# Optimization experiments

Measured on AMD Instinct MI355X. Metric: run time of the kernel, lower is better.

## Reference

```python
import math
import jax, jax.numpy as jnp
import numpy as np

NUM_HEADS = 12
HIDDEN = 768
HEAD_DIM = HIDDEN // NUM_HEADS
BS, SEQ = 4, 2048


def setup_inputs() -> dict:
    key = jax.random.key(0)
    ks = jax.random.split(key, 8)
    hidden_states = jax.random.normal(ks[0], (BS, SEQ, HIDDEN), dtype=jnp.float32)
    attention_mask = jax.random.normal(ks[1], (BS, 1, 1, SEQ), dtype=jnp.float32)
    scale = 0.02
    Wq = jax.random.normal(ks[2], (HIDDEN, HIDDEN), dtype=jnp.float32) * scale
    Wk = jax.random.normal(ks[3], (HIDDEN, HIDDEN), dtype=jnp.float32) * scale
    Wv = jax.random.normal(ks[4], (HIDDEN, HIDDEN), dtype=jnp.float32) * scale
    bq = jax.random.normal(ks[5], (HIDDEN,), dtype=jnp.float32) * scale
    bk = jax.random.normal(ks[6], (HIDDEN,), dtype=jnp.float32) * scale
    bv = jax.random.normal(ks[7], (HIDDEN,), dtype=jnp.float32) * scale
    return {"hidden_states": hidden_states, "attention_mask": attention_mask,
            "Wq": Wq, "bq": bq, "Wk": Wk, "bk": bk, "Wv": Wv, "bv": bv}


def reference(hidden_states, attention_mask, Wq, bq, Wk, bk, Wv, bv):
    B, S, H = hidden_states.shape
    nh, hd = NUM_HEADS, H // NUM_HEADS

    def transform(W, b):
        # [B,S,H] -> [B,nh,S,hd]  (nn.Linear: x @ W.T + b, then view+transpose)
        p = hidden_states @ W.T + b
        return p.reshape(B, S, nh, hd).transpose(0, 2, 1, 3)

    q = transform(Wq, bq)
    k = transform(Wk, bk)
    v = transform(Wv, bv)

    # scores: [B, nh, S, S], scaled by sqrt(head_dim)
    scores = jnp.einsum('bhqd,bhkd->bhqk', q, k) / math.sqrt(hd)
    # masked_fill(attention_mask < 0, -10000); mask broadcasts [B,1,1,S]
    scores = jnp.where(attention_mask < 0, jnp.float32(-10000.0), scores)
    probs = jax.nn.softmax(scores, axis=-1)
    per_head = jnp.einsum('bhqk,bhkd->bhqd', probs, v)
    # cat over heads along last dim == transpose back and merge head dims
    return per_head.transpose(0, 2, 1, 3).reshape(B, S, H)
```

## Files before the change

kernel.cpp:

```cpp
#include <hip/hip_runtime.h>

typedef __attribute__((ext_vector_type(8))) __bf16 bf16x8;
typedef __attribute__((ext_vector_type(4))) __bf16 bf16x4;
typedef __attribute__((ext_vector_type(4))) float f32x4;

#define NB 4
#define SEQ 2048
#define HID 768
#define NH 12
#define HD 64
#define NC 1280

#define MFMA(a,b,c) __builtin_amdgcn_mfma_f32_16x16x32_bf16(a, b, c, 0, 0, 0)

__global__ __launch_bounds__(256) void prep_kernel(
    const float* __restrict__ mask, const float* __restrict__ X,
    const float* __restrict__ Wq, const float* __restrict__ Wk,
    const float* __restrict__ Wv,
    int* __restrict__ idx, int* __restrict__ counts,
    __bf16* __restrict__ Xb, __bf16* __restrict__ Wb) {
  int blk = blockIdx.x;
  if (blk < NB) {
    int lane = threadIdx.x;
    if (lane < 64) {
      int b = blk;
      int base = 0;
      for (int c = 0; c < SEQ / 64; c++) {
        float mv = mask[b * SEQ + c * 64 + lane];
        unsigned long long ball = __ballot(mv >= 0.0f);
        int pre = __popcll(ball & ((1ull << lane) - 1ull));
        if (mv >= 0.0f) idx[b * SEQ + base + pre] = c * 64 + lane;
        base += (int)__popcll(ball);
      }
      if (lane == 0) counts[b] = base;
    }
    return;
  }
  const long NX = (long)NB * SEQ * HID;
  const long NW = (long)HID * HID;
  long i8 = ((long)(blk - NB) * 256 + threadIdx.x) * 8;
  const float* src;
  __bf16* dst;
  if (i8 < NX) {
    src = X + i8; dst = Xb + i8;
  } else {
    long j = i8 - NX;
    int w = (int)(j / NW);
    long r = j - (long)w * NW;
    src = (w == 0 ? Wq : (w == 1 ? Wk : Wv)) + r;
    dst = Wb + j;
  }
  const float4* s4 = (const float4*)src;
  float4 a = s4[0], b = s4[1];
  bf16x8 v;
  v[0] = (__bf16)a.x; v[1] = (__bf16)a.y; v[2] = (__bf16)a.z; v[3] = (__bf16)a.w;
  v[4] = (__bf16)b.x; v[5] = (__bf16)b.y; v[6] = (__bf16)b.z; v[7] = (__bf16)b.w;
  *(bf16x8*)dst = v;
}

__global__ __launch_bounds__(512) void qkv_kernel(
    const __bf16* __restrict__ Xb, const int* __restrict__ idx,
    const int* __restrict__ counts, const __bf16* __restrict__ Wb,
    const float* __restrict__ bq, const float* __restrict__ bk,
    const float* __restrict__ bv,
    __bf16* __restrict__ Qb, __bf16* __restrict__ Kc,
    __bf16* __restrict__ Vtc) {
  __shared__ alignas(16) __bf16 As[16384];
  __shared__ alignas(16) __bf16 Bs[8192];
  int tid = threadIdx.x, lane = tid & 63, wid = tid >> 6;
  int bidx = blockIdx.x;
  int w, tm, n0;
  if (bidx < 192)      { w = 0; tm = bidx / 6;          n0 = (bidx % 6) * 128; }
  else if (bidx < 312) { w = 1; tm = (bidx - 192) / 6;  n0 = ((bidx - 192) % 6) * 128; }
  else                 { w = 2; tm = (bidx - 312) / 6;  n0 = ((bidx - 312) % 6) * 128; }
  int m0 = tm * 256;
  int wm = wid >> 1, wn = wid & 1;
  int la = lane & 15, lg = lane >> 4;

  int r0 = tid >> 3, csw = (tid & 7) ^ (r0 & 7);
  long aoff[4];
  if (w == 0) {
#pragma unroll
    for (int p = 0; p < 4; p++)
      aoff[p] = (long)(m0 + p * 64 + r0) * HID + csw * 8;
  } else {
    int bI = m0 / NC, jbase = m0 - bI * NC;
    int cnt = counts[bI];
#pragma unroll
    for (int p = 0; p < 4; p++) {
      int j = jbase + p * 64 + r0;
      int src = (j < cnt) ? idx[bI * SEQ + j] : 0;
      aoff[p] = (long)(bI * SEQ + src) * HID + csw * 8;
    }
  }
  long wbase = (long)w * HID * HID;
  long boff[2];
#pragma unroll
  for (int p = 0; p < 2; p++)
    boff[p] = wbase + (long)(n0 + p * 64 + r0) * HID + csw * 8;

  int aoffL[2][4], boffL[2][4];
#pragma unroll
  for (int kk = 0; kk < 2; kk++)
#pragma unroll
    for (int i = 0; i < 4; i++) {
      int r = wm * 64 + i * 16 + la;
      aoffL[kk][i] = r * 64 + (((kk * 4 + lg) ^ (r & 7)) * 8);
      int rb = wn * 64 + i * 16 + la;
      boffL[kk][i] = rb * 64 + (((kk * 4 + lg) ^ (rb & 7)) * 8);
    }

  bf16x8 areg[4], breg[2];
#pragma unroll
  for (int p = 0; p < 4; p++) areg[p] = *(const bf16x8*)(Xb + aoff[p]);
#pragma unroll
  for (int p = 0; p < 2; p++) breg[p] = *(const bf16x8*)(Wb + boff[p]);

  f32x4 acc[4][4] = {};
  for (int kt = 0; kt < 12; kt++) {
#pragma unroll
    for (int p = 0; p < 4; p++)
      *(bf16x8*)(As + p * 4096 + tid * 8) = areg[p];
#pragma unroll
    for (int p = 0; p < 2; p++)
      *(bf16x8*)(Bs + p * 4096 + tid * 8) = breg[p];
    __syncthreads();

    long kn = (kt + 1 == 12) ? 0 : (long)(kt + 1) * 64;
#pragma unroll
    for (int p = 0; p < 4; p++) areg[p] = *(const bf16x8*)(Xb + aoff[p] + kn);
#pragma unroll
    for (int p = 0; p < 2; p++) breg[p] = *(const bf16x8*)(Wb + boff[p] + kn);

#pragma unroll
    for (int kk = 0; kk < 2; kk++) {
      bf16x8 af[4], bfv[4];
#pragma unroll
      for (int i = 0; i < 4; i++) af[i] = *(const bf16x8*)(As + aoffL[kk][i]);
#pragma unroll
      for (int j = 0; j < 4; j++) bfv[j] = *(const bf16x8*)(Bs + boffL[kk][j]);
#pragma unroll
      for (int i = 0; i < 4; i++)
#pragma unroll
        for (int j = 0; j < 4; j++)
          acc[i][j] = MFMA(af[i], bfv[j], acc[i][j]);
    }
    __syncthreads();
  }

  const float* bias = (w == 0) ? bq : ((w == 1) ? bk : bv);
  const float qscale = (w == 0) ? 0.18033688011112042f : 1.0f;
#pragma unroll
  for (int j = 0; j < 4; j++) {
    int nc = n0 + wn * 64 + j * 16 + la;
    float bb = bias[nc];
#pragma unroll
    for (int i = 0; i < 4; i++) {
      int mrow0 = m0 + wm * 64 + i * 16 + lg * 4;
      f32x4 v = acc[i][j];
      if (w < 2) {
        __bf16* dst = (w == 0 ? Qb : Kc);
#pragma unroll
        for (int reg = 0; reg < 4; reg++)
          dst[(long)(mrow0 + reg) * HID + nc] = (__bf16)((v[reg] + bb) * qscale);
      } else {
        int bI = mrow0 / NC, j0 = mrow0 - bI * NC;
        int hh = nc >> 6, d = nc & 63;
        bf16x4 pv;
#pragma unroll
        for (int reg = 0; reg < 4; reg++) pv[reg] = (__bf16)(v[reg] + bb);
        *(bf16x4*)(Vtc + ((long)(bI * NH + hh) * HD + d) * NC + j0) = pv;
      }
    }
  }
}

__global__ __launch_bounds__(512) void attn_kernel(
    const __bf16* __restrict__ Qb, const __bf16* __restrict__ Kc,
    const __bf16* __restrict__ Vtc, const int* __restrict__ counts,
    float* __restrict__ out) {
  __shared__ alignas(16) __bf16 Ks[4096];
  __shared__ alignas(16) __bf16 Vs[4096];
  __shared__ alignas(16) __bf16 Ps[8192];
  int tid = threadIdx.x, lane = tid & 63, wid = tid >> 6;
  int qt = blockIdx.x, h = blockIdx.y, b = blockIdx.z;
  int la = lane & 15, lg = lane >> 4;

  int cnt = counts[b];
  int ntiles = (cnt + 63) >> 6;

  int qrow = qt * 128 + wid * 16 + la;
  const __bf16* qp = Qb + (long)(b * SEQ + qrow) * HID + h * HD + lg * 8;
  bf16x8 qa0 = *(const bf16x8*)qp;
  bf16x8 qa1 = *(const bf16x8*)(qp + 32);

  int r0 = tid >> 3, cc = (tid & 7) ^ (r0 & 7);
  long kbase = (long)(b * NC + r0) * HID + h * HD + cc * 8;
  long vbase = ((long)(b * NH + h) * HD + r0) * NC + cc * 8;

  int koffL[4][2];
#pragma unroll
  for (int j = 0; j < 4; j++) {
    int r = j * 16 + la;
    koffL[j][0] = r * 64 + (((0 + lg) ^ (r & 7)) * 8);
    koffL[j][1] = r * 64 + (((4 + lg) ^ (r & 7)) * 8);
  }
  int poff0 = wid * 1024 + la * 64 + (((0 + lg) ^ (la & 7)) * 8);
  int poff1 = wid * 1024 + la * 64 + (((4 + lg) ^ (la & 7)) * 8);
  int psaddr[4][4];
#pragma unroll
  for (int j = 0; j < 4; j++)
#pragma unroll
    for (int r = 0; r < 4; r++) {
      int row = lg * 4 + r, col = j * 16 + la;
      psaddr[j][r] =
          wid * 1024 + row * 64 + (((col >> 3) ^ (row & 7)) * 8) + (col & 7);
    }

  float m_run[4] = {0.f, 0.f, 0.f, 0.f};
  float l_run[4] = {0.f, 0.f, 0.f, 0.f};
  f32x4 acc[4] = {};
  bf16x8 vone;
#pragma unroll
  for (int i = 0; i < 8; i++) vone[i] = (__bf16)1.0f;

  bf16x8 kreg = *(const bf16x8*)(Kc + kbase);
  bf16x8 vreg = *(const bf16x8*)(Vtc + vbase);

  for (int t = 0; t < ntiles; t++) {
    *(bf16x8*)(Ks + tid * 8) = kreg;
    *(bf16x8*)(Vs + tid * 8) = vreg;
    __syncthreads();

    int tn = (t + 1 == ntiles) ? 0 : (t + 1);
    kreg = *(const bf16x8*)(Kc + kbase + (long)tn * (64 * HID));
    vreg = *(const bf16x8*)(Vtc + vbase + tn * 64);

    f32x4 s[4];
#pragma unroll
    for (int j = 0; j < 4; j++) {
      bf16x8 k0 = *(const bf16x8*)(Ks + koffL[j][0]);
      bf16x8 k1 = *(const bf16x8*)(Ks + koffL[j][1]);
      f32x4 z = {};
      z = MFMA(qa0, k0, z);
      z = MFMA(qa1, k1, z);
      s[j] = z;
    }

    float mx[4] = {-1e30f, -1e30f, -1e30f, -1e30f};
    if ((t + 1) * 64 <= cnt) {
#pragma unroll
      for (int j = 0; j < 4; j++)
#pragma unroll
        for (int r = 0; r < 4; r++) {
          float a = s[j][r] - m_run[r];
          s[j][r] = a;
          mx[r] = fmaxf(mx[r], a);
        }
    } else {
#pragma unroll
      for (int j = 0; j < 4; j++) {
        float mneg = ((t * 64 + j * 16 + la) < cnt) ? 0.0f : -30000.0f;
#pragma unroll
        for (int r = 0; r < 4; r++) {
          float a = s[j][r] + (mneg - m_run[r]);
          s[j][r] = a;
          mx[r] = fmaxf(mx[r], a);
        }
      }
    }
    int ok = (mx[0] <= 8.f) & (mx[1] <= 8.f) & (mx[2] <= 8.f) & (mx[3] <= 8.f);
    if (__builtin_expect(!__all(ok), 0)) {
#pragma unroll
      for (int r = 0; r < 4; r++) {
        float rm = mx[r];
#pragma unroll
        for (int o = 1; o < 16; o <<= 1) rm = fmaxf(rm, __shfl_xor(rm, o, 16));
        rm = fmaxf(rm, 0.0f);
        float corr = __builtin_amdgcn_exp2f(-rm);
        m_run[r] += rm;
        l_run[r] *= corr;
#pragma unroll
        for (int jo = 0; jo < 4; jo++) acc[jo][r] *= corr;
#pragma unroll
        for (int j = 0; j < 4; j++) s[j][r] -= rm;
      }
    }

#pragma unroll
    for (int j = 0; j < 4; j++)
#pragma unroll
      for (int r = 0; r < 4; r++)
        Ps[psaddr[j][r]] = (__bf16)__builtin_amdgcn_exp2f(s[j][r]);
    bf16x8 pa0 = *(const bf16x8*)(Ps + poff0);
    bf16x8 pa1 = *(const bf16x8*)(Ps + poff1);

    f32x4 z = {};
    z = MFMA(pa0, vone, z);
    z = MFMA(pa1, vone, z);
#pragma unroll
    for (int r = 0; r < 4; r++) l_run[r] += z[r];

#pragma unroll
    for (int jo = 0; jo < 4; jo++) {
      bf16x8 v0 = *(const bf16x8*)(Vs + koffL[jo][0]);
      bf16x8 v1 = *(const bf16x8*)(Vs + koffL[jo][1]);
      acc[jo] = MFMA(pa0, v0, acc[jo]);
      acc[jo] = MFMA(pa1, v1, acc[jo]);
    }

    __syncthreads();
  }

#pragma unroll
  for (int jo = 0; jo < 4; jo++)
#pragma unroll
    for (int r = 0; r < 4; r++) {
      int row = qt * 128 + wid * 16 + lg * 4 + r;
      int d = jo * 16 + la;
      out[(long)(b * SEQ + row) * HID + h * HD + d] = acc[jo][r] / l_run[r];
    }
}

extern "C" void kernel_launch(void* const* d_in, const int* in_sizes, int n_in,
                              void* d_out, int out_size, void* d_ws, size_t ws_size,
                              hipStream_t stream) {
  const float* X    = (const float*)d_in[0];
  const float* mask = (const float*)d_in[1];
  const float* Wq   = (const float*)d_in[2];
  const float* bq   = (const float*)d_in[3];
  const float* Wk   = (const float*)d_in[4];
  const float* bk   = (const float*)d_in[5];
  const float* Wv   = (const float*)d_in[6];
  const float* bv   = (const float*)d_in[7];

  __bf16* Xb  = (__bf16*)d_ws;
  __bf16* Wb  = Xb + 6291456;
  __bf16* Qb  = Wb + 1769472;
  __bf16* Kc  = Qb + 6291456;
  __bf16* Vtc = Kc + 3932160;
  int* idx    = (int*)(Vtc + 3932160);
  int* counts = idx + NB * SEQ;
  float* out  = (float*)d_out;

  prep_kernel<<<dim3(3940), dim3(256), 0, stream>>>(mask, X, Wq, Wk, Wv,
                                                    idx, counts, Xb, Wb);
  qkv_kernel<<<dim3(432), dim3(512), 0, stream>>>(Xb, idx, counts, Wb,
                                                  bq, bk, bv, Qb, Kc, Vtc);
  attn_kernel<<<dim3(16, 12, 4), dim3(512), 0, stream>>>(Qb, Kc, Vtc, counts,
                                                         out);
}
```

Measured before the change: 97.89 us.

## Compute transposed scores so P stays in registers, dropping the LDS round-trip

The QK^T MFMA now runs with K as the A operand and Q as B, so each lane holds scores for a single query row. K rows are loaded in a permuted order so that the exponentiated probabilities already sit in the A-operand layout for the PV MFMA. This removes the shared-memory P buffer along with its scattered scalar writes and vector reads. Row-max handling collapses to a cross-lane shuffle, and the per-row correction is broadcast via shuffles, which adds some shuffle cost in the rare rescale path.

```diff
diff --git a/kernel.cpp b/kernel.cpp
--- a/kernel.cpp
+++ b/kernel.cpp
@@ -181,7 +181,6 @@
     float* __restrict__ out) {
   __shared__ alignas(16) __bf16 Ks[4096];
   __shared__ alignas(16) __bf16 Vs[4096];
-  __shared__ alignas(16) __bf16 Ps[8192];
   int tid = threadIdx.x, lane = tid & 63, wid = tid >> 6;
   int qt = blockIdx.x, h = blockIdx.y, b = blockIdx.z;
   int la = lane & 15, lg = lane >> 4;
@@ -195,7 +194,8 @@
   bf16x8 qa1 = *(const bf16x8*)(qp + 32);
 
   int r0 = tid >> 3, cc = (tid & 7) ^ (r0 & 7);
-  long kbase = (long)(b * NC + r0) * HID + h * HD + cc * 8;
+  int nu = (r0 >> 5) * 32 + ((r0 & 15) >> 2) * 8 + ((r0 >> 4) & 1) * 4 + (r0 & 3);
+  long kbase = (long)(b * NC + nu) * HID + h * HD + cc * 8;
   long vbase = ((long)(b * NH + h) * HD + r0) * NC + cc * 8;
 
   int koffL[4][2];
@@ -205,19 +205,8 @@
     koffL[j][0] = r * 64 + (((0 + lg) ^ (r & 7)) * 8);
     koffL[j][1] = r * 64 + (((4 + lg) ^ (r & 7)) * 8);
   }
-  int poff0 = wid * 1024 + la * 64 + (((0 + lg) ^ (la & 7)) * 8);
-  int poff1 = wid * 1024 + la * 64 + (((4 + lg) ^ (la & 7)) * 8);
-  int psaddr[4][4];
-#pragma unroll
-  for (int j = 0; j < 4; j++)
-#pragma unroll
-    for (int r = 0; r < 4; r++) {
-      int row = lg * 4 + r, col = j * 16 + la;
-      psaddr[j][r] =
-          wid * 1024 + row * 64 + (((col >> 3) ^ (row & 7)) * 8) + (col & 7);
-    }
-
-  float m_run[4] = {0.f, 0.f, 0.f, 0.f};
+
+  float m_run = 0.f;
   float l_run[4] = {0.f, 0.f, 0.f, 0.f};
   f32x4 acc[4] = {};
   bf16x8 vone;
@@ -238,62 +227,65 @@
 
     f32x4 s[4];
 #pragma unroll
-    for (int j = 0; j < 4; j++) {
-      bf16x8 k0 = *(const bf16x8*)(Ks + koffL[j][0]);
-      bf16x8 k1 = *(const bf16x8*)(Ks + koffL[j][1]);
+    for (int g = 0; g < 4; g++) {
+      bf16x8 k0 = *(const bf16x8*)(Ks + koffL[g][0]);
+      bf16x8 k1 = *(const bf16x8*)(Ks + koffL[g][1]);
       f32x4 z = {};
-      z = MFMA(qa0, k0, z);
-      z = MFMA(qa1, k1, z);
-      s[j] = z;
-    }
-
-    float mx[4] = {-1e30f, -1e30f, -1e30f, -1e30f};
+      z = MFMA(k0, qa0, z);
+      z = MFMA(k1, qa1, z);
+      s[g] = z;
+    }
+
+    float mx = -1e30f;
     if ((t + 1) * 64 <= cnt) {
 #pragma unroll
-      for (int j = 0; j < 4; j++)
+      for (int g = 0; g < 4; g++)
 #pragma unroll
         for (int r = 0; r < 4; r++) {
-          float a = s[j][r] - m_run[r];
-          s[j][r] = a;
-          mx[r] = fmaxf(mx[r], a);
+          float a = s[g][r] - m_run;
+          s[g][r] = a;
+          mx = fmaxf(mx, a);
         }
     } else {
 #pragma unroll
-      for (int j = 0; j < 4; j++) {
-        float mneg = ((t * 64 + j * 16 + la) < cnt) ? 0.0f : -30000.0f;
+      for (int g = 0; g < 4; g++) {
+        int kb = t * 64 + (g >> 1) * 32 + (g & 1) * 4 + lg * 8;
 #pragma unroll
         for (int r = 0; r < 4; r++) {
-          float a = s[j][r] + (mneg - m_run[r]);
-          s[j][r] = a;
-          mx[r] = fmaxf(mx[r], a);
+          float mneg = ((kb + r) < cnt) ? 0.0f : -30000.0f;
+          float a = s[g][r] + (mneg - m_run);
+          s[g][r] = a;
+          mx = fmaxf(mx, a);
         }
       }
     }
-    int ok = (mx[0] <= 8.f) & (mx[1] <= 8.f) & (mx[2] <= 8.f) & (mx[3] <= 8.f);
-    if (__builtin_expect(!__all(ok), 0)) {
+    if (__builtin_expect(!__all(mx <= 8.f), 0)) {
+      float rm = fmaxf(mx, __shfl_xor(mx, 16));
+      rm = fmaxf(rm, __shfl_xor(rm, 32));
+      rm = fmaxf(rm, 0.0f);
+      float corr = __builtin_amdgcn_exp2f(-rm);
+      m_run += rm;
 #pragma unroll
       for (int r = 0; r < 4; r++) {
-        float rm = mx[r];
-#pragma unroll
-        for (int o = 1; o < 16; o <<= 1) rm = fmaxf(rm, __shfl_xor(rm, o, 16));
-        rm = fmaxf(rm, 0.0f);
-        float corr = __builtin_amdgcn_exp2f(-rm);
-        m_run[r] += rm;
-        l_run[r] *= corr;
-#pragma unroll
-        for (int jo = 0; jo < 4; jo++) acc[jo][r] *= corr;
-#pragma unroll
-        for (int j = 0; j < 4; j++) s[j][r] -= rm;
+        float cq = __shfl(corr, lg * 4 + r, 64);
+        l_run[r] *= cq;
+#pragma unroll
+        for (int jo = 0; jo < 4; jo++) acc[jo][r] *= cq;
       }
-    }
-
-#pragma unroll
-    for (int j = 0; j < 4; j++)
-#pragma unroll
-      for (int r = 0; r < 4; r++)
-        Ps[psaddr[j][r]] = (__bf16)__builtin_amdgcn_exp2f(s[j][r]);
-    bf16x8 pa0 = *(const bf16x8*)(Ps + poff0);
-    bf16x8 pa1 = *(const bf16x8*)(Ps + poff1);
+#pragma unroll
+      for (int g = 0; g < 4; g++)
+#pragma unroll
+        for (int r = 0; r < 4; r++) s[g][r] -= rm;
+    }
+
+    bf16x8 pa0, pa1;
+#pragma unroll
+    for (int r = 0; r < 4; r++) {
+      pa0[r]     = (__bf16)__builtin_amdgcn_exp2f(s[0][r]);
+      pa0[4 + r] = (__bf16)__builtin_amdgcn_exp2f(s[1][r]);
+      pa1[r]     = (__bf16)__builtin_amdgcn_exp2f(s[2][r]);
+      pa1[4 + r] = (__bf16)__builtin_amdgcn_exp2f(s[3][r]);
+    }
 
     f32x4 z = {};
     z = MFMA(pa0, vone, z);
```

New measurement: 92.90 us (median of 3 runs). 5.1% less time.
